# Optimization experiments

Measured on AMD Instinct MI355X. Metric: run time of the kernel, lower is better.

The kernel has to match this reference:

```python
import jax, jax.numpy as jnp
import numpy as np


def setup_inputs() -> dict:
    key = jax.random.key(0)
    k1, k2, k3, k4, k5 = jax.random.split(key, 5)
    B, C, D = 16384, 1000, 2048
    x = jax.random.normal(k1, (B, D), dtype=jnp.float32)
    W = jax.random.normal(k2, (C, D), dtype=jnp.float32) * 0.02  # fc weight
    b = jax.random.normal(k3, (C,), dtype=jnp.float32) * 0.01
    selector_weights = jax.random.normal(k4, (5,), dtype=jnp.float32) * 0.01
    selector_thresholds = jax.random.normal(k5, (5,), dtype=jnp.float32) * 0.01
    ensemble_threshold = jnp.zeros((1,), dtype=jnp.float32)
    return {
        "x": x, "W": W, "b": b,
        "selector_weights": selector_weights,
        "selector_thresholds": selector_thresholds,
        "ensemble_threshold": ensemble_threshold,
    }


def _selector_scores(logits, W):
    # top-2 of raw logits (RLConfM): sorted descending -> top_k(2)
    top2, _ = jax.lax.top_k(logits, 2)
    conf_m = top2[:, 0] - top2[:, 1]
    # geometric margin (RLGeoM): logits normalized by row norms of fc weight
    w_norms = jnp.linalg.norm(W, axis=1)                      # [C]
    norm_logits = logits / (w_norms + 1e-8)[None, :]          # [B, C]
    ntop2, _ = jax.lax.top_k(norm_logits, 2)
    geo_m = ntop2[:, 0] - ntop2[:, 1]
    # softmax-based selectors share one softmax pass
    probs = jax.nn.softmax(logits, axis=1)                    # [B, C]
    sr_max = jnp.max(probs, axis=1)
    doctor = 1.0 - 1.0 / jnp.sum(probs * probs, axis=1)
    neg_entropy = jnp.sum(probs * jnp.log(probs + 1e-10), axis=1)  # = -entropy
    # order matches nn.ModuleList: [SRMax, SRDoctor, SREntropy, RLGeoM, RLConfM]
    return jnp.stack([sr_max, doctor, neg_entropy, geo_m, conf_m], axis=1)  # [B, 5]


def reference(x, W, b, selector_weights, selector_thresholds, ensemble_threshold):
    # base model runs under no_grad in the original
    logits = jax.lax.stop_gradient(jnp.dot(x, W.T) + b)       # [B, C]
    scores = _selector_scores(logits, jax.lax.stop_gradient(W))  # [B, 5]
    indicators = jnp.tanh(scores - selector_thresholds[None, :])  # [B, 5]
    ensemble = jnp.sum(selector_weights[None, :] * indicators, axis=1)  # [B]
    selection_score = jnp.tanh(ensemble - ensemble_threshold[0])
    return (logits, selection_score)
```

## Files before the change

### kernel.cpp

```cpp
#include <hip/hip_runtime.h>
#include <stdint.h>

#define B_ROWS 16384
#define C_COLS 1000
#define D_DIM  2048

typedef __bf16 bf16x8 __attribute__((ext_vector_type(8)));
typedef float  f32x4  __attribute__((ext_vector_type(4)));
typedef unsigned short u16;

__device__ __forceinline__ u16 f2bf(float f) {
  union { float f; uint32_t u; } v; v.f = f;
  return (u16)((v.u + 0x7FFFu + ((v.u >> 16) & 1u)) >> 16);
}

__global__ __launch_bounds__(256)
void prep(const float* __restrict__ W, const float* __restrict__ x,
          u16* __restrict__ Wb, u16* __restrict__ xb, float* __restrict__ norms) {
  const int r = blockIdx.x;
  const int t = threadIdx.x;
  const bool isW = (r < C_COLS);
  const float* src = isW ? (W + (size_t)r * D_DIM)
                         : (x + (size_t)(r - C_COLS) * D_DIM);
  u16* dst = isW ? (Wb + (size_t)r * D_DIM)
                 : (xb + (size_t)(r - C_COLS) * D_DIM);
  const int c = t * 8;
  float4 v0 = *reinterpret_cast<const float4*>(src + c);
  float4 v1 = *reinterpret_cast<const float4*>(src + c + 4);
  uint32_t p0 = (uint32_t)f2bf(v0.x) | ((uint32_t)f2bf(v0.y) << 16);
  uint32_t p1 = (uint32_t)f2bf(v0.z) | ((uint32_t)f2bf(v0.w) << 16);
  uint32_t p2 = (uint32_t)f2bf(v1.x) | ((uint32_t)f2bf(v1.y) << 16);
  uint32_t p3 = (uint32_t)f2bf(v1.z) | ((uint32_t)f2bf(v1.w) << 16);
  const int row_id = isW ? r : (r - C_COLS);
  const int m2 = (row_id & 7) << 3;
  uint4 val; val.x = p0; val.y = p1; val.z = p2; val.w = p3;
  *reinterpret_cast<uint4*>(dst + (c ^ m2)) = val;
  if (isW) {
    float ss = v0.x*v0.x + v0.y*v0.y + v0.z*v0.z + v0.w*v0.w
             + v1.x*v1.x + v1.y*v1.y + v1.z*v1.z + v1.w*v1.w;
    #pragma unroll
    for (int m = 32; m; m >>= 1) ss += __shfl_xor(ss, m);
    __shared__ float wss[4];
    if ((t & 63) == 0) wss[t >> 6] = ss;
    __syncthreads();
    if (t == 0) norms[r] = sqrtf(wss[0] + wss[1] + wss[2] + wss[3]);
  }
}

#define ABASE(B,H) (((B)*2+(H))*8192)
#define BBASE(B,H) (32768 + ((B)*2+(H))*8192)

#define STAGE_A(BUF,H,KT) { _Pragma("unroll") for (int j_=0;j_<2;++j_){ \
    const char* s_ = (const char*)xb + \
      (((size_t)(m0+(H)*128+j_*64+w*8+(l>>3)))*D_DIM + (KT)*64 + (l&7)*8)*2; \
    u16* d_ = lds + ABASE(BUF,H) + (j_*64 + w*8)*64; \
    __builtin_amdgcn_global_load_lds( \
      (const __attribute__((address_space(1))) void*)s_, \
      (__attribute__((address_space(3))) void*)d_, 16, 0, 0); } }

#define STAGE_B(BUF,H,KT) { _Pragma("unroll") for (int j_=0;j_<2;++j_){ \
    int gr_ = n0+(H)*128+j_*64+w*8+(l>>3); if (gr_ >= C_COLS) gr_ = C_COLS-1; \
    const char* s_ = (const char*)Wb + \
      (((size_t)gr_)*D_DIM + (KT)*64 + (l&7)*8)*2; \
    u16* d_ = lds + BBASE(BUF,H) + (j_*64 + w*8)*64; \
    __builtin_amdgcn_global_load_lds( \
      (const __attribute__((address_space(1))) void*)s_, \
      (__attribute__((address_space(3))) void*)d_, 16, 0, 0); } }

#define READ_A(BUF,MH) { _Pragma("unroll") for (int ks_=0;ks_<2;++ks_) \
  _Pragma("unroll") for (int fr_=0;fr_<4;++fr_){ \
    int ra_ = wr*64 + fr_*16 + (l&15); \
    int ca_ = (ks_*32 + ((l>>4)<<3)) ^ ((ra_&7)<<3); \
    Acur[ks_][fr_] = *reinterpret_cast<const bf16x8*>( \
        &lds[ABASE(BUF,MH) + ra_*64 + ca_]); } }

#define READ_B(BUF,NH,DST) { _Pragma("unroll") for (int ks_=0;ks_<2;++ks_) \
  _Pragma("unroll") for (int fc_=0;fc_<2;++fc_){ \
    int rb_ = wcn*32 + fc_*16 + (l&15); \
    int cb_ = (ks_*32 + ((l>>4)<<3)) ^ ((rb_&7)<<3); \
    DST[ks_][fc_] = *reinterpret_cast<const bf16x8*>( \
        &lds[BBASE(BUF,NH) + rb_*64 + cb_]); } }

#define MMA(MH,NH,BSRC) { \
  __builtin_amdgcn_s_setprio(1); \
  _Pragma("unroll") for (int ks_=0;ks_<2;++ks_) \
    _Pragma("unroll") for (int fr_=0;fr_<4;++fr_) \
      _Pragma("unroll") for (int fc_=0;fc_<2;++fc_) \
        acc[MH][fr_][NH][fc_] = __builtin_amdgcn_mfma_f32_16x16x32_bf16( \
            Acur[ks_][fr_], BSRC[ks_][fc_], acc[MH][fr_][NH][fc_], 0, 0, 0); \
  __builtin_amdgcn_s_setprio(0); }

#define BAR  __builtin_amdgcn_s_barrier()
#define LG0  asm volatile("s_waitcnt lgkmcnt(0)" ::: "memory")
#define LG8  asm volatile("s_waitcnt lgkmcnt(8)" ::: "memory")
#define SCHB __builtin_amdgcn_sched_barrier(0)
#define VM4  asm volatile("s_waitcnt vmcnt(4)" ::: "memory")
#define VM0  asm volatile("s_waitcnt vmcnt(0)" ::: "memory")

#define SMERGE(m_,s_,q_,u_,om_,os_,oq_,ou_) { \
    float M_ = fmaxf(m_, om_); \
    float a_ = __expf(m_ - M_), b_ = __expf(om_ - M_); \
    float ns_ = a_*s_ + b_*os_; \
    float nq_ = a_*a_*q_ + b_*b_*oq_; \
    float nu_ = a_*(u_ + (m_-M_)*s_) + b_*(ou_ + (om_-M_)*os_); \
    m_ = M_; s_ = ns_; q_ = nq_; u_ = nu_; }

#define T2MERGE(t1_,t2_,o1_,o2_) { \
    if (o1_ > t1_) { t2_ = fmaxf(t1_, o2_); t1_ = o1_; } else t2_ = fmaxf(t2_, o1_); }

template<int FUSE>
__global__ __launch_bounds__(512, 2)
void gemm8(const u16* __restrict__ xb, const u16* __restrict__ Wb,
           const float* __restrict__ bias, float* __restrict__ out,
           const float* __restrict__ norms, float* __restrict__ partials) {
  __shared__ u16 lds[65536];

  const int bid = blockIdx.x;
  const int swz = (bid & 7) * 32 + (bid >> 3);
  const int tm = swz >> 2, tn = swz & 3;
  const int m0 = tm * 256, n0 = tn * 256;

  const int t = threadIdx.x, w = t >> 6, l = t & 63;
  const int wr = w >> 2, wcn = w & 3;

  f32x4 acc[2][4][2][2];
  #pragma unroll
  for (int a = 0; a < 2; ++a)
    #pragma unroll
    for (int b2 = 0; b2 < 4; ++b2)
      #pragma unroll
      for (int c2 = 0; c2 < 2; ++c2)
        #pragma unroll
        for (int d2 = 0; d2 < 2; ++d2)
          acc[a][b2][c2][d2] = (f32x4){0.f, 0.f, 0.f, 0.f};

  bf16x8 Acur[2][4], B0c[2][2], B1c[2][2];

  STAGE_A(0,0,0); STAGE_B(0,0,0); STAGE_A(0,1,0); STAGE_B(0,1,0);
  STAGE_A(1,0,1); STAGE_B(1,0,1);
  VM4;
  BAR;

  for (int it = 0; it < 15; ++it) {
    const int t1k = 2*it + 1, t2k = 2*it + 2, t3k = 2*it + 3;
    READ_A(0,0); READ_B(0,0,B0c); STAGE_A(1,1,t1k); LG8;
    BAR; LG0; SCHB; MMA(0,0,B0c); BAR;
    READ_B(0,1,B1c); STAGE_B(1,1,t1k);
    BAR; LG0; SCHB; MMA(0,1,B1c); BAR;
    READ_A(0,1); STAGE_A(0,0,t2k);
    BAR; LG0; SCHB; MMA(1,1,B1c); BAR;
    STAGE_B(0,0,t2k);
    BAR; SCHB; MMA(1,0,B0c); VM4; BAR;
    READ_A(1,0); READ_B(1,0,B0c); STAGE_A(0,1,t2k); LG8;
    BAR; LG0; SCHB; MMA(0,0,B0c); BAR;
    READ_B(1,1,B1c); STAGE_B(0,1,t2k);
    BAR; LG0; SCHB; MMA(0,1,B1c); BAR;
    READ_A(1,1); STAGE_A(1,0,t3k);
    BAR; LG0; SCHB; MMA(1,1,B1c); BAR;
    STAGE_B(1,0,t3k);
    BAR; SCHB; MMA(1,0,B0c); VM4; BAR;
  }
  READ_A(0,0); READ_B(0,0,B0c); STAGE_A(1,1,31); LG8;
  BAR; LG0; SCHB; MMA(0,0,B0c); BAR;
  READ_B(0,1,B1c); STAGE_B(1,1,31);
  BAR; LG0; SCHB; MMA(0,1,B1c); BAR;
  READ_A(0,1);
  BAR; LG0; SCHB; MMA(1,1,B1c); BAR;
  BAR; SCHB; MMA(1,0,B0c); VM0; BAR;
  READ_A(1,0); READ_B(1,0,B0c); LG8;
  BAR; LG0; SCHB; MMA(0,0,B0c); BAR;
  READ_B(1,1,B1c);
  BAR; LG0; SCHB; MMA(0,1,B1c); BAR;
  READ_A(1,1);
  BAR; LG0; SCHB; MMA(1,1,B1c); BAR;
  SCHB; MMA(1,0,B0c);

  float bv[2][2]; bool okc[2][2];
  #pragma unroll
  for (int nh = 0; nh < 2; ++nh)
    #pragma unroll
    for (int fc = 0; fc < 2; ++fc) {
      int col = n0 + nh*128 + wcn*32 + fc*16 + (l & 15);
      okc[nh][fc] = (col < C_COLS);
      bv[nh][fc]  = okc[nh][fc] ? bias[col] : 0.f;
    }

  #pragma unroll
  for (int mh = 0; mh < 2; ++mh)
    #pragma unroll
    for (int nh = 0; nh < 2; ++nh)
      #pragma unroll
      for (int fc = 0; fc < 2; ++fc)
        if (okc[nh][fc]) {
          int col = n0 + nh*128 + wcn*32 + fc*16 + (l & 15);
          #pragma unroll
          for (int fr = 0; fr < 4; ++fr) {
            int row0 = m0 + mh*128 + wr*64 + fr*16 + ((l >> 4) << 2);
            #pragma unroll
            for (int j = 0; j < 4; ++j)
              out[(size_t)(row0 + j) * C_COLS + col] = acc[mh][fr][nh][fc][j] + bv[nh][fc];
          }
        }

  if constexpr (FUSE) {
    float* sf = (float*)lds;
    const int rrow = t >> 2;
    const int q    = t & 3;
    BAR;
    #pragma unroll
    for (int mh = 0; mh < 2; ++mh) {
      #pragma unroll
      for (int fr = 0; fr < 4; ++fr)
        #pragma unroll
        for (int j = 0; j < 4; ++j) {
          int rl = wr*64 + fr*16 + ((l >> 4) << 2) + j;
          int sw = (rl & 7) << 2;
          #pragma unroll
          for (int nh = 0; nh < 2; ++nh)
            #pragma unroll
            for (int fc = 0; fc < 2; ++fc) {
              int c = nh*128 + wcn*32 + fc*16 + (l & 15);
              sf[rl*256 + (c ^ sw)] = acc[mh][fr][nh][fc][j] + bv[nh][fc];
            }
        }
      LG0; BAR;
      float m=-3.4e38f, t1=-3.4e38f, t2=-3.4e38f, n1=-3.4e38f, n2=-3.4e38f;
      #pragma unroll
      for (int i = 0; i < 16; ++i) {
        int U = q*16 + i;
        f32x4 v4 = *reinterpret_cast<const f32x4*>(
            &sf[rrow*256 + 4*(U ^ (rrow & 7))]);
        f32x4 w4 = *reinterpret_cast<const f32x4*>(&norms[n0 + 4*U]);
        #pragma unroll
        for (int e = 0; e < 4; ++e) {
          int col = n0 + 4*U + e;
          if (col < C_COLS) {
            float v = v4[e];
            m = fmaxf(m, v);
            if (v > t1) { t2 = t1; t1 = v; } else if (v > t2) t2 = v;
            float nv = v / (w4[e] + 1e-8f);
            if (nv > n1) { n2 = n1; n1 = nv; } else if (nv > n2) n2 = nv;
          }
        }
      }
      float s = 0.f, qq = 0.f, u = 0.f;
      #pragma unroll
      for (int i = 0; i < 16; ++i) {
        int U = q*16 + i;
        f32x4 v4 = *reinterpret_cast<const f32x4*>(
            &sf[rrow*256 + 4*(U ^ (rrow & 7))]);
        #pragma unroll
        for (int e = 0; e < 4; ++e) {
          int col = n0 + 4*U + e;
          if (col < C_COLS) {
            float d = v4[e] - m;
            float ee = __expf(d);
            s += ee; qq += ee*ee; u += d*ee;
          }
        }
      }
      LG0;
      #pragma unroll
      for (int msk = 1; msk < 4; msk <<= 1) {
        float o1 = __shfl_xor(t1, msk), o2 = __shfl_xor(t2, msk);
        T2MERGE(t1, t2, o1, o2);
        float p1 = __shfl_xor(n1, msk), p2 = __shfl_xor(n2, msk);
        T2MERGE(n1, n2, p1, p2);
        float om = __shfl_xor(m, msk), os = __shfl_xor(s, msk);
        float oq = __shfl_xor(qq, msk), ou = __shfl_xor(u, msk);
        SMERGE(m, s, qq, u, om, os, oq, ou);
      }
      if (q == 0) {
        float* pp = partials + ((size_t)(m0 + mh*128 + rrow) * 4 + tn) * 8;
        float4 lo; lo.x=t1; lo.y=t2; lo.z=n1; lo.w=n2;
        float4 hi; hi.x=m;  hi.y=s;  hi.z=qq; hi.w=u;
        *reinterpret_cast<float4*>(pp)     = lo;
        *reinterpret_cast<float4*>(pp + 4) = hi;
      }
      if (mh == 0) { BAR; }
    }
  }
}

__global__ __launch_bounds__(256)
void selector2(const float* __restrict__ partials,
               const float* __restrict__ selw, const float* __restrict__ selt,
               const float* __restrict__ ethr, float* __restrict__ out2) {
  const int row = blockIdx.x * 256 + threadIdx.x;
  const float* pp = partials + (size_t)row * 32;
  float P[4][8];
  #pragma unroll
  for (int wv = 0; wv < 4; ++wv) {
    float4 lo = *reinterpret_cast<const float4*>(pp + wv*8);
    float4 hi = *reinterpret_cast<const float4*>(pp + wv*8 + 4);
    P[wv][0]=lo.x; P[wv][1]=lo.y; P[wv][2]=lo.z; P[wv][3]=lo.w;
    P[wv][4]=hi.x; P[wv][5]=hi.y; P[wv][6]=hi.z; P[wv][7]=hi.w;
  }
  float t1=P[0][0], t2=P[0][1], n1=P[0][2], n2=P[0][3];
  float m=P[0][4], s=P[0][5], q=P[0][6], u=P[0][7];
  #pragma unroll
  for (int wv = 1; wv < 4; ++wv) {
    T2MERGE(t1, t2, P[wv][0], P[wv][1]);
    T2MERGE(n1, n2, P[wv][2], P[wv][3]);
    SMERGE(m, s, q, u, P[wv][4], P[wv][5], P[wv][6], P[wv][7]);
  }
  float sc0 = 1.f / s;
  float sc1 = 1.f - (s * s) / q;
  float sc2 = u / s - __logf(s);
  float sc3 = n1 - n2;
  float sc4 = t1 - t2;
  float ens = selw[0] * tanhf(sc0 - selt[0])
            + selw[1] * tanhf(sc1 - selt[1])
            + selw[2] * tanhf(sc2 - selt[2])
            + selw[3] * tanhf(sc3 - selt[3])
            + selw[4] * tanhf(sc4 - selt[4]);
  out2[row] = tanhf(ens - ethr[0]);
}

__global__ __launch_bounds__(256)
void selector(const float* __restrict__ logits, const float* __restrict__ norms,
              const float* __restrict__ selw, const float* __restrict__ selt,
              const float* __restrict__ ethr, float* __restrict__ out) {
  __shared__ float nrm[1024];
  const int t = threadIdx.x;
  #pragma unroll
  for (int i = 0; i < 4; ++i) {
    int idx = t + i * 256;
    nrm[idx] = (idx < C_COLS) ? norms[idx] : 1.0f;
  }
  __syncthreads();
  const int w = t >> 6, l = t & 63;
  const int row = blockIdx.x * 4 + w;
  const float* lp = logits + (size_t)row * C_COLS;
  float lg[16];
  float t1 = -3.4e38f, t2 = -3.4e38f, n1 = -3.4e38f, n2 = -3.4e38f;
  #pragma unroll
  for (int i = 0; i < 4; ++i) {
    float4 v4 = *reinterpret_cast<const float4*>(lp + l * 4 + i * 256);
    #pragma unroll
    for (int j = 0; j < 4; ++j) {
      int idx = l * 4 + i * 256 + j;
      float raw = (j == 0) ? v4.x : (j == 1) ? v4.y : (j == 2) ? v4.z : v4.w;
      bool ok = (idx < C_COLS);
      float v = ok ? raw : -3.4e38f;
      lg[i * 4 + j] = v;
      if (v > t1) { t2 = t1; t1 = v; } else if (v > t2) t2 = v;
      float nv = ok ? raw / (nrm[idx] + 1e-8f) : -3.4e38f;
      if (nv > n1) { n2 = n1; n1 = nv; } else if (nv > n2) n2 = nv;
    }
  }
  #pragma unroll
  for (int m = 1; m < 64; m <<= 1) {
    float o1 = __shfl_xor(t1, m), o2 = __shfl_xor(t2, m);
    T2MERGE(t1, t2, o1, o2);
    float p1 = __shfl_xor(n1, m), p2 = __shfl_xor(n2, m);
    T2MERGE(n1, n2, p1, p2);
  }
  const float mx = t1;
  float S = 0.f, sq = 0.f;
  float ex[16];
  #pragma unroll
  for (int i = 0; i < 16; ++i) {
    float e = (lg[i] > -1e38f) ? __expf(lg[i] - mx) : 0.f;
    ex[i] = e; S += e; sq += e * e;
  }
  #pragma unroll
  for (int m = 1; m < 64; m <<= 1) { S += __shfl_xor(S, m); sq += __shfl_xor(sq, m); }
  float ent = 0.f;
  #pragma unroll
  for (int i = 0; i < 16; ++i)
    if (lg[i] > -1e38f) { float p = ex[i] / S; ent += p * __logf(p + 1e-10f); }
  #pragma unroll
  for (int m = 1; m < 64; m <<= 1) ent += __shfl_xor(ent, m);
  if (l == 0) {
    float ens = selw[0] * tanhf(1.f / S - selt[0])
              + selw[1] * tanhf(1.f - (S * S) / sq - selt[1])
              + selw[2] * tanhf(ent - selt[2])
              + selw[3] * tanhf(n1 - n2 - selt[3])
              + selw[4] * tanhf(t1 - t2 - selt[4]);
    out[row] = tanhf(ens - ethr[0]);
  }
}

extern "C" void kernel_launch(void* const* d_in, const int* in_sizes, int n_in,
                              void* d_out, int out_size, void* d_ws, size_t ws_size,
                              hipStream_t stream) {
  const float* x    = (const float*)d_in[0];
  const float* W    = (const float*)d_in[1];
  const float* b    = (const float*)d_in[2];
  const float* selw = (const float*)d_in[3];
  const float* selt = (const float*)d_in[4];
  const float* ethr = (const float*)d_in[5];
  float* out = (float*)d_out;
  float* out2 = out + (size_t)B_ROWS * C_COLS;

  u16*   Wb    = (u16*)d_ws;
  float* norms = (float*)((char*)d_ws + 4096000);
  u16*   xb    = (u16*)((char*)d_ws + 4100096);
  float* parts = (float*)((char*)d_ws + 4100096 + 67108864);

  const size_t need_fuse = 4100096 + 67108864 + 2097152;
  const size_t need_r4   = 4100096 + 67108864;

  if (ws_size >= need_fuse) {
    prep<<<C_COLS + B_ROWS, 256, 0, stream>>>(W, x, Wb, xb, norms);
    gemm8<1><<<256, 512, 0, stream>>>(xb, Wb, b, out, norms, parts);
    selector2<<<B_ROWS / 256, 256, 0, stream>>>(parts, selw, selt, ethr, out2);
  } else if (ws_size >= need_r4) {
    prep<<<C_COLS + B_ROWS, 256, 0, stream>>>(W, x, Wb, xb, norms);
    gemm8<0><<<256, 512, 0, stream>>>(xb, Wb, b, out, norms, nullptr);
    selector<<<B_ROWS / 4, 256, 0, stream>>>(out, norms, selw, selt, ethr, out2);
  }
}
```

Baseline: 126.8 us.

## Merge GEMM pipeline phases to halve barrier count per k-iteration

```diff
diff --git a/kernel.cpp b/kernel.cpp
--- a/kernel.cpp
+++ b/kernel.cpp
@@ -143,37 +143,26 @@
 
   for (int it = 0; it < 15; ++it) {
     const int t1k = 2*it + 1, t2k = 2*it + 2, t3k = 2*it + 3;
-    READ_A(0,0); READ_B(0,0,B0c); STAGE_A(1,1,t1k); LG8;
-    BAR; LG0; SCHB; MMA(0,0,B0c); BAR;
-    READ_B(0,1,B1c); STAGE_B(1,1,t1k);
-    BAR; LG0; SCHB; MMA(0,1,B1c); BAR;
-    READ_A(0,1); STAGE_A(0,0,t2k);
-    BAR; LG0; SCHB; MMA(1,1,B1c); BAR;
-    STAGE_B(0,0,t2k);
-    BAR; SCHB; MMA(1,0,B0c); VM4; BAR;
-    READ_A(1,0); READ_B(1,0,B0c); STAGE_A(0,1,t2k); LG8;
-    BAR; LG0; SCHB; MMA(0,0,B0c); BAR;
-    READ_B(1,1,B1c); STAGE_B(0,1,t2k);
-    BAR; LG0; SCHB; MMA(0,1,B1c); BAR;
-    READ_A(1,1); STAGE_A(1,0,t3k);
-    BAR; LG0; SCHB; MMA(1,1,B1c); BAR;
-    STAGE_B(1,0,t3k);
-    BAR; SCHB; MMA(1,0,B0c); VM4; BAR;
-  }
-  READ_A(0,0); READ_B(0,0,B0c); STAGE_A(1,1,31); LG8;
-  BAR; LG0; SCHB; MMA(0,0,B0c); BAR;
-  READ_B(0,1,B1c); STAGE_B(1,1,31);
-  BAR; LG0; SCHB; MMA(0,1,B1c); BAR;
+    READ_A(0,0); READ_B(0,0,B0c); READ_B(0,1,B1c);
+    STAGE_A(1,1,t1k); STAGE_B(1,1,t1k); LG8;
+    BAR; LG0; SCHB; MMA(0,0,B0c); MMA(0,1,B1c); BAR;
+    READ_A(0,1); STAGE_A(0,0,t2k); STAGE_B(0,0,t2k);
+    BAR; LG0; SCHB; MMA(1,1,B1c); MMA(1,0,B0c); VM4; BAR;
+    READ_A(1,0); READ_B(1,0,B0c); READ_B(1,1,B1c);
+    STAGE_A(0,1,t2k); STAGE_B(0,1,t2k); LG8;
+    BAR; LG0; SCHB; MMA(0,0,B0c); MMA(0,1,B1c); BAR;
+    READ_A(1,1); STAGE_A(1,0,t3k); STAGE_B(1,0,t3k);
+    BAR; LG0; SCHB; MMA(1,1,B1c); MMA(1,0,B0c); VM4; BAR;
+  }
+  READ_A(0,0); READ_B(0,0,B0c); READ_B(0,1,B1c);
+  STAGE_A(1,1,31); STAGE_B(1,1,31); LG8;
+  BAR; LG0; SCHB; MMA(0,0,B0c); MMA(0,1,B1c); BAR;
   READ_A(0,1);
-  BAR; LG0; SCHB; MMA(1,1,B1c); BAR;
-  BAR; SCHB; MMA(1,0,B0c); VM0; BAR;
-  READ_A(1,0); READ_B(1,0,B0c); LG8;
-  BAR; LG0; SCHB; MMA(0,0,B0c); BAR;
-  READ_B(1,1,B1c);
-  BAR; LG0; SCHB; MMA(0,1,B1c); BAR;
+  BAR; LG0; SCHB; MMA(1,1,B1c); MMA(1,0,B0c); VM0; BAR;
+  READ_A(1,0); READ_B(1,0,B0c); READ_B(1,1,B1c); LG8;
+  BAR; LG0; SCHB; MMA(0,0,B0c); MMA(0,1,B1c); BAR;
   READ_A(1,1);
-  BAR; LG0; SCHB; MMA(1,1,B1c); BAR;
-  SCHB; MMA(1,0,B0c);
+  BAR; LG0; SCHB; MMA(1,1,B1c); MMA(1,0,B0c);
 
   float bv[2][2]; bool okc[2][2];
   #pragma unroll
```

Result: no change. 126.4 us (-0.3%).
